# Optimization experiments

Hardware: AMD Instinct MI355X
Metric: run time of the kernel (lower is better)

Reference implementation:

```python
import jax, jax.numpy as jnp
import numpy as np

NB_COMP = 8
LAT_DIM = 512
NB_NEUR = 1024
OUT_DIM = 512
N_SAMPLES = 16384


def setup_inputs() -> dict:
    key = jax.random.key(0)
    ks = jax.random.split(key, 8)
    s1 = 1.0 / np.sqrt(LAT_DIM)
    s2 = 1.0 / np.sqrt(NB_NEUR)
    return {
        "epsilon": jax.random.normal(ks[0], (N_SAMPLES, LAT_DIM), dtype=jnp.float32),
        "comp_idx": jax.random.randint(ks[1], (N_SAMPLES,), 0, NB_COMP, dtype=jnp.int32),
        "mu": jnp.zeros((NB_COMP, LAT_DIM), dtype=jnp.float32),
        "rho": jnp.zeros((NB_COMP,), dtype=jnp.float32),  # sigma = softplus(rho)
        "W1": jax.random.normal(ks[2], (NB_COMP, LAT_DIM, NB_NEUR), dtype=jnp.float32) * s1,
        "b1": jax.random.normal(ks[3], (NB_COMP, NB_NEUR), dtype=jnp.float32) * s1,
        "W2": jax.random.normal(ks[4], (NB_COMP, NB_NEUR, OUT_DIM), dtype=jnp.float32) * s2,
        "b2": jax.random.normal(ks[5], (NB_COMP, OUT_DIM), dtype=jnp.float32) * s2,
    }


def reference(epsilon, comp_idx, mu, rho, W1, b1, W2, b2):
    # GNNens.forward: per-sample categorical component dispatch through a
    # 1-hidden-layer sigmoid MLP. Vectorized as compute-all-components + select.
    sigma = jax.nn.softplus(rho)                          # [C]
    # lat_c[c,n,d] = epsilon[n,d] * sigma[c] + mu[c,d]
    lat = epsilon[None, :, :] * sigma[:, None, None] + mu[:, None, :]  # [C,N,D]
    h = jax.nn.sigmoid(jnp.einsum('cnd,cdh->cnh', lat, W1) + b1[:, None, :])  # [C,N,H]
    y = jnp.einsum('cnh,cho->cno', h, W2) + b2[:, None, :]                    # [C,N,O]
    # select each sample's routed component
    idx = comp_idx[None, :, None].astype(jnp.int32)       # [1,N,1]
    out = jnp.take_along_axis(y, idx, axis=0)[0]          # [N,O]
    return out
```

## Files before the change

kernel.cpp:

```cpp
#include <hip/hip_runtime.h>
#include <stdint.h>

#define NCOMP 8
#define LATD  512
#define HID   1024
#define OUTD  512
#define NS    16384

typedef unsigned short u16;
typedef __bf16 bf16x8 __attribute__((ext_vector_type(8)));
typedef float  f32x4  __attribute__((ext_vector_type(4)));

#define MAPS       (NS/128 + NCOMP)
#define SLOT_CHUNK ((MAPS + 7)/8)

#define ORDER_OFF  2048
#define APACK_OFF  (ORDER_OFF + NS*4)
#define W1T_OFF    (APACK_OFF + (size_t)NS*LATD*2)
#define W2T_OFF    (W1T_OFF + (size_t)NCOMP*LATD*HID*2)
#define H_OFF      (W2T_OFF + (size_t)NCOMP*HID*OUTD*2)
#define WS_NEEDED  (H_OFF + (size_t)NS*HID*2)

__device__ __forceinline__ u16 f2b(float f) {
  unsigned int u = __builtin_bit_cast(unsigned int, f);
  u = (u + 0x7FFFu + ((u >> 16) & 1u)) >> 16;
  return (u16)u;
}

__device__ __forceinline__ void load_lds16(const void* g, void* l) {
  __builtin_amdgcn_global_load_lds((const __attribute__((address_space(1))) void*)g,
                                   (__attribute__((address_space(3))) void*)l, 16, 0, 0);
}

__global__ __launch_bounds__(1024)
void k_prep_all(const int* __restrict__ idx, const float* __restrict__ rho,
                const float* __restrict__ eps, const float* __restrict__ mu,
                const float* __restrict__ W1, const float* __restrict__ W2,
                int* __restrict__ offsets, int* __restrict__ ntiles,
                int* __restrict__ map, int* __restrict__ order,
                u16* __restrict__ Apack, u16* __restrict__ W1T, u16* __restrict__ W2T) {
  __shared__ float tile[64][65];
  __shared__ int hist_s[NCOMP];
  __shared__ int wtot[16];
  const int b = blockIdx.x;
  const int t = threadIdx.x;

  if (b < NCOMP) {
    const int c = b;
    const int wave = t >> 6, lane = t & 63;

    int my[16];
    #pragma unroll
    for (int i = 0; i < 16; ++i) my[i] = idx[t + (i << 10)];

    unsigned long long nib = 0;
    #pragma unroll
    for (int i = 0; i < 16; ++i) nib += 1ull << (my[i] << 2);

    if (t < NCOMP) hist_s[t] = 0;
    __syncthreads();

    #pragma unroll
    for (int cc = 0; cc < NCOMP; ++cc) {
      int v = (int)((nib >> (cc << 2)) & 15);
      #pragma unroll
      for (int d = 1; d < 64; d <<= 1) v += __shfl_xor(v, d);
      if (lane == 0) atomicAdd(&hist_s[cc], v);
    }

    int v = (int)((nib >> (c << 2)) & 15);
    int s = v;
    #pragma unroll
    for (int d = 1; d < 64; d <<= 1) {
      int u = __shfl_up(s, d);
      if (lane >= d) s += u;
    }
    if (lane == 63) wtot[wave] = s;
    __syncthreads();

    int wbase = 0;
    for (int w = 0; w < wave; ++w) wbase += wtot[w];
    int off_c = 0;
    #pragma unroll
    for (int cc = 0; cc < NCOMP; ++cc) if (cc < c) off_c += hist_s[cc];

    int pos = off_c + wbase + (s - v);
    #pragma unroll
    for (int i = 0; i < 16; ++i)
      if (my[i] == c) order[pos++] = t + (i << 10);

    if (t == 0) {
      if (c == 0) {
        int a = 0;
        for (int cc = 0; cc < NCOMP; ++cc) { offsets[cc] = a; a += hist_s[cc]; }
        offsets[NCOMP] = a;
        int tot = 0;
        for (int cc = 0; cc < NCOMP; ++cc) tot += (hist_s[cc] + 127) >> 7;
        ntiles[0] = tot;
      }
      int mb = 0;
      for (int cc = 0; cc < c; ++cc) mb += (hist_s[cc] + 127) >> 7;
      int nt = (hist_s[c] + 127) >> 7;
      for (int m = 0; m < nt; ++m) map[mb + m] = (c << 16) | m;
    }
  } else if (b < NCOMP + 1024) {
    int g = (b - NCOMP) * 1024 + t;
    int i = g >> 6;
    int d = (g & 63) << 3;
    int c = idx[i];
    float r = rho[c];
    float sg = (r > 20.f) ? r : log1pf(expf(r));
    const float4* ep = reinterpret_cast<const float4*>(eps + (size_t)i*LATD + d);
    const float4* mp = reinterpret_cast<const float4*>(mu  + (size_t)c*LATD + d);
    float4 e0 = ep[0], e1 = ep[1], m0 = mp[0], m1 = mp[1];
    unsigned o0 = f2b(e0.x*sg+m0.x), o1 = f2b(e0.y*sg+m0.y), o2 = f2b(e0.z*sg+m0.z), o3 = f2b(e0.w*sg+m0.w);
    unsigned o4 = f2b(e1.x*sg+m1.x), o5 = f2b(e1.y*sg+m1.y), o6 = f2b(e1.z*sg+m1.z), o7 = f2b(e1.w*sg+m1.w);
    uint4 pk;
    pk.x = o0 | (o1<<16); pk.y = o2 | (o3<<16); pk.z = o4 | (o5<<16); pk.w = o6 | (o7<<16);
    *reinterpret_cast<uint4*>(Apack + (size_t)i*LATD + d) = pk;
  } else {
    int bb = b - (NCOMP + 1024);
    const float* src; u16* dst; int CC, r0, c0;
    int R;
    if (bb < 1024) {
      int comp = bb >> 7, loc = bb & 127;
      R = LATD; CC = HID;
      c0 = (loc & 15) << 6; r0 = (loc >> 4) << 6;
      src = W1 + (size_t)comp*R*CC; dst = W1T + (size_t)comp*R*CC;
    } else {
      int b2 = bb - 1024;
      int comp = b2 >> 7, loc = b2 & 127;
      R = HID; CC = OUTD;
      c0 = (loc & 7) << 6; r0 = (loc >> 3) << 6;
      src = W2 + (size_t)comp*R*CC; dst = W2T + (size_t)comp*R*CC;
    }
    int tx = t & 63, ty = t >> 6;
    for (int rr = ty; rr < 64; rr += 16)
      tile[rr][tx] = src[(size_t)(r0+rr)*CC + c0 + tx];
    __syncthreads();
    for (int rr = ty; rr < 64; rr += 16)
      dst[(size_t)(c0+rr)*R + r0 + tx] = f2b(tile[tx][rr]);
  }
}

template<int K, int NB, int STAGE>
__global__ __launch_bounds__(256, 4)
void k_gemm(const u16* __restrict__ A, const u16* __restrict__ BT,
            const int* __restrict__ offsets, const int* __restrict__ ntiles,
            const int* __restrict__ map, const int* __restrict__ order,
            const float* __restrict__ bias,
            u16* __restrict__ Hout, float* __restrict__ Yout) {
  constexpr int NCB = NB/128;
  __shared__ u16 As[128*64];
  __shared__ u16 Bs[128*64];
  __shared__ int ord[128];

  const int id    = blockIdx.x;
  const int xcd   = id & 7;
  const int sub   = id >> 3;
  const int ncolb = sub % NCB;
  const int slot  = xcd*SLOT_CHUNK + sub / NCB;
  if (slot >= ntiles[0]) return;
  const int packed = map[slot];
  const int c      = packed >> 16;
  const int bstart = offsets[c];
  const int bend   = offsets[c+1];
  const int tile0  = bstart + (packed & 0xffff)*128;
  const int ncol0  = ncolb*128;

  const int tid  = threadIdx.x;
  const int wave = tid >> 6;
  const int lane = tid & 63;
  const int srow = (wave<<5) + (lane>>3);
  const int scol = ((lane & 7) ^ ((lane >> 3) & 7)) << 3;

  if (STAGE == 2 && tid < 128) {
    int gr = tile0 + tid;
    ord[tid] = order[gr < bend ? gr : bstart];
  }

  size_t a_off[4], b_off[4];
  const size_t bbase = (size_t)c * NB * K;
  #pragma unroll
  for (int i = 0; i < 4; ++i) {
    int ar = tile0 + srow + (i<<3);
    if (ar >= bend) ar = bend - 1;
    int arow = (STAGE == 1) ? order[ar] : ar;
    a_off[i] = (size_t)arow * K + scol;
    b_off[i] = bbase + (size_t)(ncol0 + srow + (i<<3)) * K + scol;
  }

  const int wr   = (wave >> 1) << 6;
  const int wc   = (wave & 1) << 6;
  const int quad = lane >> 4;
  const int l16  = lane & 15;
  const int sw   = l16 & 7;

  float bcol[4];
  #pragma unroll
  for (int ni = 0; ni < 4; ++ni)
    bcol[ni] = bias[(size_t)c*NB + ncol0 + wc + (ni<<4) + l16];

  f32x4 acc[4][4] = {};

  for (int k0 = 0; k0 < K; k0 += 64) {
    #pragma unroll
    for (int i = 0; i < 4; ++i)
      load_lds16(A + a_off[i] + k0, &As[((wave<<5) + (i<<3))<<6]);
    #pragma unroll
    for (int i = 0; i < 4; ++i)
      load_lds16(BT + b_off[i] + k0, &Bs[((wave<<5) + (i<<3))<<6]);
    __syncthreads();
    #pragma unroll
    for (int kk = 0; kk < 64; kk += 32) {
      const int kc = (kk >> 3) + quad;
      const int sc = (kc ^ sw) << 3;
      bf16x8 af[4], bfr[4];
      #pragma unroll
      for (int mi = 0; mi < 4; ++mi)
        af[mi] = *reinterpret_cast<const bf16x8*>(&As[((wr + (mi<<4) + l16)<<6) + sc]);
      #pragma unroll
      for (int ni = 0; ni < 4; ++ni)
        bfr[ni] = *reinterpret_cast<const bf16x8*>(&Bs[((wc + (ni<<4) + l16)<<6) + sc]);
      #pragma unroll
      for (int mi = 0; mi < 4; ++mi)
        #pragma unroll
        for (int ni = 0; ni < 4; ++ni)
          acc[mi][ni] = __builtin_amdgcn_mfma_f32_16x16x32_bf16(af[mi], bfr[ni], acc[mi][ni], 0, 0, 0);
    }
    __syncthreads();
  }

  #pragma unroll
  for (int mi = 0; mi < 4; ++mi) {
    #pragma unroll
    for (int r = 0; r < 4; ++r) {
      const int row_l = wr + (mi<<4) + (quad<<2) + r;
      const int grow  = tile0 + row_l;
      if (grow < bend) {
        #pragma unroll
        for (int ni = 0; ni < 4; ++ni) {
          const int col = ncol0 + wc + (ni<<4) + l16;
          float v = acc[mi][ni][r] + bcol[ni];
          if (STAGE == 1) {
            v = 1.0f / (1.0f + __expf(-v));
            Hout[(size_t)grow*NB + col] = f2b(v);
          } else {
            Yout[(size_t)ord[row_l]*NB + col] = v;
          }
        }
      }
    }
  }
}

__global__ void k_naive(const float* __restrict__ eps, const int* __restrict__ idx,
                        const float* __restrict__ mu, const float* __restrict__ rho,
                        const float* __restrict__ W1, const float* __restrict__ b1,
                        const float* __restrict__ W2, const float* __restrict__ b2,
                        float* __restrict__ out) {
  __shared__ float lat[LATD];
  __shared__ float h[HID];
  int n = blockIdx.x, t = threadIdx.x;
  int c = idx[n];
  float r = rho[c];
  float sg = (r > 20.f) ? r : log1pf(expf(r));
  for (int d = t; d < LATD; d += 256) lat[d] = eps[(size_t)n*LATD+d]*sg + mu[(size_t)c*LATD+d];
  __syncthreads();
  for (int j = t; j < HID; j += 256) {
    float a = b1[(size_t)c*HID+j];
    const float* w = W1 + (size_t)c*LATD*HID + j;
    for (int d = 0; d < LATD; ++d) a += lat[d]*w[(size_t)d*HID];
    h[j] = 1.f/(1.f+expf(-a));
  }
  __syncthreads();
  for (int o = t; o < OUTD; o += 256) {
    float a = b2[(size_t)c*OUTD+o];
    const float* w = W2 + (size_t)c*HID*OUTD + o;
    for (int j = 0; j < HID; ++j) a += h[j]*w[(size_t)j*OUTD];
    out[(size_t)n*OUTD+o] = a;
  }
}

extern "C" void kernel_launch(void* const* d_in, const int* in_sizes, int n_in,
                              void* d_out, int out_size, void* d_ws, size_t ws_size,
                              hipStream_t stream) {
  const float* eps = (const float*)d_in[0];
  const int*   idx = (const int*)d_in[1];
  const float* mu  = (const float*)d_in[2];
  const float* rho = (const float*)d_in[3];
  const float* W1  = (const float*)d_in[4];
  const float* b1  = (const float*)d_in[5];
  const float* W2  = (const float*)d_in[6];
  const float* b2  = (const float*)d_in[7];
  float* out = (float*)d_out;

  if (ws_size < WS_NEEDED) {
    k_naive<<<NS, 256, 0, stream>>>(eps, idx, mu, rho, W1, b1, W2, b2, out);
    return;
  }

  char* ws = (char*)d_ws;
  int*   offsets = (int*)(ws + 0);
  int*   ntiles  = (int*)(ws + 96);
  int*   map     = (int*)(ws + 128);
  int*   order   = (int*)(ws + ORDER_OFF);
  u16*   Apack   = (u16*)(ws + APACK_OFF);
  u16*   W1T     = (u16*)(ws + W1T_OFF);
  u16*   W2T     = (u16*)(ws + W2T_OFF);
  u16*   Hws     = (u16*)(ws + H_OFF);

  k_prep_all<<<NCOMP + 1024 + 2048, 1024, 0, stream>>>(
      idx, rho, eps, mu, W1, W2, offsets, ntiles, map, order, Apack, W1T, W2T);
  k_gemm<LATD, HID, 1><<<8*SLOT_CHUNK*(HID/128), 256, 0, stream>>>(
      Apack, W1T, offsets, ntiles, map, order, b1, Hws, nullptr);
  k_gemm<HID, OUTD, 2><<<8*SLOT_CHUNK*(OUTD/128), 256, 0, stream>>>(
      Hws, W2T, offsets, ntiles, map, order, b2, nullptr, out);
}
```

Measured before the change: 178.4 us.

## Stage GEMM epilogues through LDS for vectorized coalesced stores and pack transpose writes

Both GEMM epilogues now write accumulator results into a padded shared-memory tile, then issue 16-byte coalesced row stores to global memory instead of scattered 2- or 4-byte column writes. The sigmoid uses a hardware reciprocal. The weight transpose kernel now packs four bf16 values per 8-byte store. The aim is to cut global store transactions, at the cost of extra LDS traffic, extra barriers and a larger shared-memory footprint that could affect occupancy.

Measured after the change: 190.2 us. 1.07x slower.

```diff
diff --git a/kernel.cpp b/kernel.cpp
--- a/kernel.cpp
+++ b/kernel.cpp
@@ -138,10 +138,19 @@
     for (int rr = ty; rr < 64; rr += 16)
       tile[rr][tx] = src[(size_t)(r0+rr)*CC + c0 + tx];
     __syncthreads();
-    for (int rr = ty; rr < 64; rr += 16)
-      dst[(size_t)(c0+rr)*R + r0 + tx] = f2b(tile[tx][rr]);
-  }
-}
+    int cc = t >> 4, ch = t & 15;
+    float f0 = tile[(ch<<2)+0][cc];
+    float f1 = tile[(ch<<2)+1][cc];
+    float g2 = tile[(ch<<2)+2][cc];
+    float g3 = tile[(ch<<2)+3][cc];
+    uint2 pk;
+    pk.x = (unsigned)f2b(f0) | ((unsigned)f2b(f1) << 16);
+    pk.y = (unsigned)f2b(g2) | ((unsigned)f2b(g3) << 16);
+    *reinterpret_cast<uint2*>(&dst[(size_t)(c0+cc)*R + r0 + (ch<<2)]) = pk;
+  }
+}
+
+#define SMEM_BYTES 34816
 
 template<int K, int NB, int STAGE>
 __global__ __launch_bounds__(256, 4)
@@ -151,9 +160,10 @@
             const float* __restrict__ bias,
             u16* __restrict__ Hout, float* __restrict__ Yout) {
   constexpr int NCB = NB/128;
-  __shared__ u16 As[128*64];
-  __shared__ u16 Bs[128*64];
+  __shared__ __align__(16) char smem[SMEM_BYTES];
   __shared__ int ord[128];
+  u16* As = (u16*)smem;
+  u16* Bs = (u16*)(smem + 16384);
 
   const int id    = blockIdx.x;
   const int xcd   = id & 7;
@@ -231,25 +241,65 @@
     __syncthreads();
   }
 
-  #pragma unroll
-  for (int mi = 0; mi < 4; ++mi) {
-    #pragma unroll
-    for (int r = 0; r < 4; ++r) {
-      const int row_l = wr + (mi<<4) + (quad<<2) + r;
+  if (STAGE == 1) {
+    u16* Ct = (u16*)smem;
+    #pragma unroll
+    for (int mi = 0; mi < 4; ++mi) {
+      const int row0 = wr + (mi<<4) + (quad<<2);
+      #pragma unroll
+      for (int ni = 0; ni < 4; ++ni) {
+        const int col = wc + (ni<<4) + l16;
+        #pragma unroll
+        for (int r = 0; r < 4; ++r) {
+          float v = acc[mi][ni][r] + bcol[ni];
+          float e = __expf(-v);
+          v = __builtin_amdgcn_rcpf(1.0f + e);
+          Ct[(row0 + r)*136 + col] = f2b(v);
+        }
+      }
+    }
+    __syncthreads();
+    #pragma unroll
+    for (int j = 0; j < 8; ++j) {
+      const int idx2  = tid + (j<<8);
+      const int row_l = idx2 >> 4;
+      const int ch    = idx2 & 15;
       const int grow  = tile0 + row_l;
       if (grow < bend) {
+        uint4 v = *reinterpret_cast<const uint4*>(&Ct[row_l*136 + (ch<<3)]);
+        *reinterpret_cast<uint4*>(&Hout[(size_t)grow*NB + ncol0 + (ch<<3)]) = v;
+      }
+    }
+  } else {
+    float* Ft = (float*)smem;
+    #pragma unroll
+    for (int h = 0; h < 2; ++h) {
+      if ((wr >> 6) == h) {
         #pragma unroll
-        for (int ni = 0; ni < 4; ++ni) {
-          const int col = ncol0 + wc + (ni<<4) + l16;
-          float v = acc[mi][ni][r] + bcol[ni];
-          if (STAGE == 1) {
-            v = 1.0f / (1.0f + __expf(-v));
-            Hout[(size_t)grow*NB + col] = f2b(v);
-          } else {
-            Yout[(size_t)ord[row_l]*NB + col] = v;
+        for (int mi = 0; mi < 4; ++mi) {
+          const int row0 = (mi<<4) + (quad<<2);
+          #pragma unroll
+          for (int ni = 0; ni < 4; ++ni) {
+            const int col = wc + (ni<<4) + l16;
+            #pragma unroll
+            for (int r = 0; r < 4; ++r)
+              Ft[(row0 + r)*132 + col] = acc[mi][ni][r] + bcol[ni];
           }
         }
       }
+      __syncthreads();
+      #pragma unroll
+      for (int j = 0; j < 8; ++j) {
+        const int idx2  = tid + (j<<8);
+        const int row_l = idx2 >> 5;
+        const int ch    = idx2 & 31;
+        const int gr    = tile0 + (h<<6) + row_l;
+        if (gr < bend) {
+          float4 v = *reinterpret_cast<const float4*>(&Ft[row_l*132 + (ch<<2)]);
+          *reinterpret_cast<float4*>(&Yout[(size_t)ord[(h<<6)+row_l]*NB + ncol0 + (ch<<2)]) = v;
+        }
+      }
+      __syncthreads();
     }
   }
 }
```
